# Performance work log

Hardware: AMD Instinct MI355X
Metric: run time of the kernel (lower is better)

Reference implementation:

```python
import jax, jax.numpy as jnp
import numpy as np

BETA = 0.01  # commitment loss weight


def setup_inputs() -> dict:
    key = jax.random.key(0)
    k1, k2 = jax.random.split(key)
    B, D, K, L = 65536, 128, 256, 4
    x = jax.random.normal(k1, (B, D), dtype=jnp.float32)
    # L codebooks, each [K, D]
    codebooks = jax.random.normal(k2, (L, K, D), dtype=jnp.float32) * 0.1
    return {"x": x, "codebooks": codebooks}


def reference(x, codebooks):
    """Residual VQ: sequentially quantize the residual against each codebook.

    x: [B, D], codebooks: [L, K, D]
    Returns (hard_indices [B,L] int, soft_probs [B,K,L], quantized [B,D], quant_losses [B,L]).
    """
    sg = jax.lax.stop_gradient

    def step(residual, cb):  # residual: [B, D], cb: [K, D]
        # squared euclidean distances [B, K] (cdist^2), expanded to avoid [B,K,D] intermediate
        d = (jnp.sum(residual * residual, axis=-1, keepdims=True)
             - 2.0 * residual @ cb.T
             + jnp.sum(cb * cb, axis=-1))
        idx = jnp.argmin(d, axis=-1)                      # [B]
        probs = jax.nn.softmax(-d, axis=-1)               # [B, K] soft assignment
        q = cb[idx]                                       # [B, D] nearest codes
        # per-sample VQ loss: codebook + beta * commitment (mean over D)
        loss = (jnp.mean((sg(residual) - q) ** 2, axis=-1)
                + BETA * jnp.mean((residual - sg(q)) ** 2, axis=-1))  # [B]
        # straight-through estimator
        q_st = residual + sg(q - residual)                # [B, D]
        return residual - q_st, (idx, probs, q_st, loss)

    _, (idxs, probs, quants, losses) = jax.lax.scan(step, x, codebooks)
    hard_indices = jnp.moveaxis(idxs, 0, -1)    # [B, L]
    soft_probs = jnp.moveaxis(probs, 0, -1)     # [B, K, L] (torch.stack(..., dim=-1))
    quantized = jnp.sum(quants, axis=0)         # [B, D]
    quant_losses = jnp.moveaxis(losses, 0, -1)  # [B, L]
    return hard_indices, soft_probs, quantized, quant_losses
```

## Files before the change

kernel.cpp:

```cpp
#include <hip/hip_runtime.h>
#include <math.h>

#define Bq 65536
#define Dd 128
#define Kk 256
#define Ll 4

constexpr int BR = 64;
constexpr int THREADS = 256;
constexpr int DC = 16;

constexpr size_t OUT_IDX   = 0;
constexpr size_t OUT_PROBS = (size_t)Bq * Ll;
constexpr size_t OUT_QUANT = OUT_PROBS + (size_t)Bq * Kk * Ll;
constexpr size_t OUT_LOSS  = OUT_QUANT + (size_t)Bq * Dd;

__global__ void cc_kernel(const float* __restrict__ cb, float* __restrict__ cc) {
  int k = blockIdx.x * blockDim.x + threadIdx.x;
  const float4* row = (const float4*)(cb + (size_t)k * Dd);
  float s = 0.f;
#pragma unroll
  for (int i = 0; i < Dd / 4; ++i) {
    float4 v = row[i];
    s += v.x * v.x + v.y * v.y + v.z * v.z + v.w * v.w;
  }
  cc[k] = s;
}

__launch_bounds__(THREADS)
__global__ void rvq_kernel(const float* __restrict__ x, const float* __restrict__ cb,
                           const float* __restrict__ cc, float* __restrict__ out) {
  __shared__ float r_lds[BR][Dd];
  __shared__ float cb_lds[Kk][DC];
  __shared__ float cc_lds[Kk];

  const int t  = threadIdx.x;
  const int tx = t & 31;
  const int ty = t >> 5;
  const int brow = blockIdx.x * BR;

  {
    const float4* xs = (const float4*)(x + (size_t)brow * Dd);
    float4* rd = (float4*)&r_lds[0][0];
#pragma unroll
    for (int i = 0; i < 8; ++i) rd[t + i * THREADS] = xs[t + i * THREADS];
  }
  __syncthreads();

  float rr_reg[8];
#pragma unroll
  for (int i = 0; i < 8; ++i) {
    float4 v = *(const float4*)&r_lds[ty * 8 + i][tx * 4];
    float s = v.x * v.x;
    s = fmaf(v.y, v.y, s); s = fmaf(v.z, v.z, s); s = fmaf(v.w, v.w, s);
#pragma unroll
    for (int mask = 16; mask >= 1; mask >>= 1) s += __shfl_xor(s, mask, 64);
    rr_reg[i] = s;
  }

  for (int l = 0; l < Ll; ++l) {
    __syncthreads();
    cc_lds[t] = cc[l * Kk + t];

    float acc[8][8];
#pragma unroll
    for (int i = 0; i < 8; ++i)
#pragma unroll
      for (int j = 0; j < 8; ++j) acc[i][j] = 0.f;

    const float* cbl = cb + (size_t)l * Kk * Dd;

    for (int dc = 0; dc < Dd / DC; ++dc) {
      {
        const int k0 = t >> 2, dd4 = t & 3;
#pragma unroll
        for (int r = 0; r < 4; ++r) {
          int k = k0 + r * 64;
          float4 v = *(const float4*)(cbl + (size_t)k * Dd + dc * DC + dd4 * 4);
          int slot = dd4 ^ ((k >> 1) & 3);
          *(float4*)&cb_lds[k][slot * 4] = v;
        }
      }
      __syncthreads();
#pragma unroll
      for (int dd4 = 0; dd4 < 4; ++dd4) {
        float4 rv[8], cv[8];
#pragma unroll
        for (int i = 0; i < 8; ++i)
          rv[i] = *(const float4*)&r_lds[ty * 8 + i][dc * DC + dd4 * 4];
#pragma unroll
        for (int j = 0; j < 8; ++j) {
          int code = tx + 32 * j;
          int slot = dd4 ^ ((code >> 1) & 3);
          cv[j] = *(const float4*)&cb_lds[code][slot * 4];
        }
#pragma unroll
        for (int i = 0; i < 8; ++i)
#pragma unroll
          for (int j = 0; j < 8; ++j) {
            acc[i][j] = fmaf(rv[i].x, cv[j].x, acc[i][j]);
            acc[i][j] = fmaf(rv[i].y, cv[j].y, acc[i][j]);
            acc[i][j] = fmaf(rv[i].z, cv[j].z, acc[i][j]);
            acc[i][j] = fmaf(rv[i].w, cv[j].w, acc[i][j]);
          }
      }
      __syncthreads();
    }

#pragma unroll
    for (int i = 0; i < 8; ++i) {
      const int row = ty * 8 + i;
      float d[8];
      float m = 1e30f; int mi = 0;
#pragma unroll
      for (int j = 0; j < 8; ++j) {
        int code = tx + 32 * j;
        d[j] = fmaf(-2.f, acc[i][j], rr_reg[i]) + cc_lds[code];
        if (d[j] < m) { m = d[j]; mi = code; }
      }
#pragma unroll
      for (int mask = 16; mask >= 1; mask >>= 1) {
        float om = __shfl_xor(m, mask, 64);
        int  omi = __shfl_xor(mi, mask, 64);
        if (om < m || (om == m && omi < mi)) { m = om; mi = omi; }
      }
      float p[8]; float ssum = 0.f;
#pragma unroll
      for (int j = 0; j < 8; ++j) { p[j] = __expf(m - d[j]); ssum += p[j]; }
#pragma unroll
      for (int mask = 16; mask >= 1; mask >>= 1) ssum += __shfl_xor(ssum, mask, 64);
      float inv = 1.f / ssum;

      size_t pbase = OUT_PROBS + (size_t)(brow + row) * (Kk * Ll) + (size_t)l * Kk;
#pragma unroll
      for (int j = 0; j < 8; ++j) out[pbase + tx + 32 * j] = p[j] * inv;

      if (tx == 0) out[OUT_IDX + (size_t)(brow + row) * Ll + l] = (float)mi;

      float4 qv = *(const float4*)(cbl + (size_t)mi * Dd + tx * 4);
      float4 rv = *(float4*)&r_lds[row][tx * 4];
      rv.x -= qv.x; rv.y -= qv.y; rv.z -= qv.z; rv.w -= qv.w;
      *(float4*)&r_lds[row][tx * 4] = rv;
      float sq = rv.x * rv.x;
      sq = fmaf(rv.y, rv.y, sq); sq = fmaf(rv.z, rv.z, sq); sq = fmaf(rv.w, rv.w, sq);
#pragma unroll
      for (int mask = 16; mask >= 1; mask >>= 1) sq += __shfl_xor(sq, mask, 64);
      rr_reg[i] = sq;
      if (tx == 0)
        out[OUT_LOSS + (size_t)(brow + row) * Ll + l] = 1.01f * sq * (1.f / 128.f);
    }
  }

  __syncthreads();
  {
    const float4* xs = (const float4*)(x + (size_t)brow * Dd);
    float4* outq = (float4*)(out + OUT_QUANT + (size_t)brow * Dd);
    const float4* rd = (const float4*)&r_lds[0][0];
#pragma unroll
    for (int i = 0; i < 8; ++i) {
      float4 xv = xs[t + i * THREADS];
      float4 rv = rd[t + i * THREADS];
      float4 q = { xv.x - rv.x, xv.y - rv.y, xv.z - rv.z, xv.w - rv.w };
      outq[t + i * THREADS] = q;
    }
  }

  float* tr = &r_lds[0][0];
  for (int g = 0; g < 8; ++g) {
    __syncthreads();
#pragma unroll
    for (int i = 0; i < 8; ++i) {
      int f4  = t + i * THREADS;
      int row = f4 >> 8;
      int off = f4 & 255;
      float4 v = *(const float4*)&out[OUT_PROBS + (size_t)(brow + g * 8 + row) * 1024 + off * 4];
      *(float4*)&tr[row * 1024 + off * 4] = v;
    }
    __syncthreads();
#pragma unroll
    for (int i = 0; i < 8; ++i) {
      int task = t + i * THREADS;
      int row  = task >> 8;
      int k    = task & 255;
      float4 o = { tr[row * 1024 + 0 * 256 + k], tr[row * 1024 + 1 * 256 + k],
                   tr[row * 1024 + 2 * 256 + k], tr[row * 1024 + 3 * 256 + k] };
      *(float4*)&out[OUT_PROBS + (size_t)(brow + g * 8 + row) * 1024 + (size_t)k * 4] = o;
    }
  }
}

extern "C" void kernel_launch(void* const* d_in, const int* in_sizes, int n_in,
                              void* d_out, int out_size, void* d_ws, size_t ws_size,
                              hipStream_t stream) {
  const float* x  = (const float*)d_in[0];
  const float* cb = (const float*)d_in[1];
  float* out = (float*)d_out;
  float* cc  = (float*)d_ws;

  cc_kernel<<<dim3((Ll * Kk) / 256), dim3(256), 0, stream>>>(cb, cc);
  rvq_kernel<<<dim3(Bq / BR), dim3(THREADS), 0, stream>>>(x, cb, cc, out);
}
```

Before: 840.4 us.

## Double-buffer codebook tiles via direct global-to-LDS loads; split transpose kernel

Codebook chunks are now staged into a double-buffered LDS tile with async global_load_lds instructions. The next chunk is prefetched while the current one feeds the FMA loop, which removes one barrier per chunk and the register round-trip for staging. The swizzle is preserved by permuting the global source addresses. The probability transpose epilogue moves into a separate kernel, adding a launch and a separate pass over the probs buffer. The larger LDS footprint may lower occupancy.

```diff
diff --git a/kernel.cpp b/kernel.cpp
--- a/kernel.cpp
+++ b/kernel.cpp
@@ -1,4 +1,5 @@
 #include <hip/hip_runtime.h>
+#include <stdint.h>
 #include <math.h>
 
 #define Bq 65536
@@ -15,6 +16,12 @@
 constexpr size_t OUT_QUANT = OUT_PROBS + (size_t)Bq * Kk * Ll;
 constexpr size_t OUT_LOSS  = OUT_QUANT + (size_t)Bq * Dd;
 
+__device__ __forceinline__ void gload_lds16(const float* g, float* l) {
+  __builtin_amdgcn_global_load_lds(
+      (const __attribute__((address_space(1))) unsigned int*)g,
+      (__attribute__((address_space(3))) unsigned int*)l, 16, 0, 0);
+}
+
 __global__ void cc_kernel(const float* __restrict__ cb, float* __restrict__ cc) {
   int k = blockIdx.x * blockDim.x + threadIdx.x;
   const float4* row = (const float4*)(cb + (size_t)k * Dd);
@@ -31,12 +38,14 @@
 __global__ void rvq_kernel(const float* __restrict__ x, const float* __restrict__ cb,
                            const float* __restrict__ cc, float* __restrict__ out) {
   __shared__ float r_lds[BR][Dd];
-  __shared__ float cb_lds[Kk][DC];
+  __shared__ float cb_lds[2][Kk][DC];
   __shared__ float cc_lds[Kk];
 
-  const int t  = threadIdx.x;
-  const int tx = t & 31;
-  const int ty = t >> 5;
+  const int t    = threadIdx.x;
+  const int tx   = t & 31;
+  const int ty   = t >> 5;
+  const int wv   = t >> 6;
+  const int lane = t & 63;
   const int brow = blockIdx.x * BR;
 
   {
@@ -59,8 +68,23 @@
   }
 
   for (int l = 0; l < Ll; ++l) {
+    const float* cbl = cb + (size_t)l * Kk * Dd;
+
+    auto stage = [&](int b, int dc) {
+#pragma unroll
+      for (int q = 0; q < 4; ++q) {
+        int region = wv * 4 + q;
+        int k      = region * 16 + (lane >> 2);
+        int slot   = lane & 3;
+        int dd4s   = slot ^ ((k >> 1) & 3);
+        const float* g = cbl + (size_t)k * Dd + dc * DC + dd4s * 4;
+        gload_lds16(g, &cb_lds[b][0][0] + region * 256);
+      }
+    };
+
+    cc_lds[t] = cc[l * Kk + t];
+    stage(0, 0);
     __syncthreads();
-    cc_lds[t] = cc[l * Kk + t];
 
     float acc[8][8];
 #pragma unroll
@@ -68,20 +92,9 @@
 #pragma unroll
       for (int j = 0; j < 8; ++j) acc[i][j] = 0.f;
 
-    const float* cbl = cb + (size_t)l * Kk * Dd;
-
     for (int dc = 0; dc < Dd / DC; ++dc) {
-      {
-        const int k0 = t >> 2, dd4 = t & 3;
-#pragma unroll
-        for (int r = 0; r < 4; ++r) {
-          int k = k0 + r * 64;
-          float4 v = *(const float4*)(cbl + (size_t)k * Dd + dc * DC + dd4 * 4);
-          int slot = dd4 ^ ((k >> 1) & 3);
-          *(float4*)&cb_lds[k][slot * 4] = v;
-        }
-      }
-      __syncthreads();
+      if (dc < Dd / DC - 1) stage((dc + 1) & 1, dc + 1);
+      const int b = dc & 1;
 #pragma unroll
       for (int dd4 = 0; dd4 < 4; ++dd4) {
         float4 rv[8], cv[8];
@@ -92,7 +105,7 @@
         for (int j = 0; j < 8; ++j) {
           int code = tx + 32 * j;
           int slot = dd4 ^ ((code >> 1) & 3);
-          cv[j] = *(const float4*)&cb_lds[code][slot * 4];
+          cv[j] = *(const float4*)&cb_lds[b][code][slot * 4];
         }
 #pragma unroll
         for (int i = 0; i < 8; ++i)
@@ -164,16 +177,21 @@
       outq[t + i * THREADS] = q;
     }
   }
-
-  float* tr = &r_lds[0][0];
+}
+
+__launch_bounds__(THREADS)
+__global__ void tr_kernel(float* __restrict__ out) {
+  __shared__ float tr[8 * 1024];
+  const int t = threadIdx.x;
+  const size_t brow = (size_t)blockIdx.x * BR;
   for (int g = 0; g < 8; ++g) {
-    __syncthreads();
+    if (g) __syncthreads();
 #pragma unroll
     for (int i = 0; i < 8; ++i) {
       int f4  = t + i * THREADS;
       int row = f4 >> 8;
       int off = f4 & 255;
-      float4 v = *(const float4*)&out[OUT_PROBS + (size_t)(brow + g * 8 + row) * 1024 + off * 4];
+      float4 v = *(const float4*)&out[OUT_PROBS + (brow + g * 8 + row) * 1024 + off * 4];
       *(float4*)&tr[row * 1024 + off * 4] = v;
     }
     __syncthreads();
@@ -184,7 +202,7 @@
       int k    = task & 255;
       float4 o = { tr[row * 1024 + 0 * 256 + k], tr[row * 1024 + 1 * 256 + k],
                    tr[row * 1024 + 2 * 256 + k], tr[row * 1024 + 3 * 256 + k] };
-      *(float4*)&out[OUT_PROBS + (size_t)(brow + g * 8 + row) * 1024 + (size_t)k * 4] = o;
+      *(float4*)&out[OUT_PROBS + (brow + g * 8 + row) * 1024 + (size_t)k * 4] = o;
     }
   }
 }
@@ -199,4 +217,5 @@
 
   cc_kernel<<<dim3((Ll * Kk) / 256), dim3(256), 0, stream>>>(cb, cc);
   rvq_kernel<<<dim3(Bq / BR), dim3(THREADS), 0, stream>>>(x, cb, cc, out);
-}
+  tr_kernel<<<dim3(Bq / BR), dim3(THREADS), 0, stream>>>(out);
+}
```

After: 813.1 us. 1.03x faster.
